# Optimization experiments

Measured on AMD Instinct MI355X. Metric: run time of the kernel, lower is better.

## Reference

```python
import jax, jax.numpy as jnp
import numpy as np

B, T, D = 2, 4096, 512
H = 8
HD = D // H  # 64


def setup_inputs() -> dict:
    key = jax.random.key(0)
    k1, k2, k3 = jax.random.split(key, 3)
    x = jax.random.normal(k1, (B, T, D), dtype=jnp.float32)
    w_qkv = jax.random.normal(k2, (3 * D, D), dtype=jnp.float32) * (1.0 / np.sqrt(D))
    w_out = jax.random.normal(k3, (D, D), dtype=jnp.float32) * (1.0 / np.sqrt(D))
    return {"x": x, "w_qkv": w_qkv, "w_out": w_out}


def reference(x, w_qkv, w_out):
    b, t, d = x.shape
    qkv = x @ w_qkv.T                      # [B,T,3D]
    q, k, v = jnp.split(qkv, 3, axis=-1)
    # b t (h d) -> b h t d
    def split_heads(a):
        return a.reshape(b, t, H, HD).transpose(0, 2, 1, 3)
    q, k, v = split_heads(q), split_heads(k), split_heads(v)
    scale = 1.0 / np.sqrt(HD).astype(np.float32)
    scores = jnp.einsum('bhqd,bhkd->bhqk', q, k) * scale  # [B,H,T,T]
    causal = jnp.tril(jnp.ones((t, t), dtype=bool))        # keep lower triangle
    scores = jnp.where(causal[None, None], scores, -jnp.inf)
    attn = jax.nn.softmax(scores, axis=-1)
    out = jnp.einsum('bhqk,bhkd->bhqd', attn, v)           # [B,H,T,HD]
    out = out.transpose(0, 2, 1, 3).reshape(b, t, d)       # b h t d -> b t (h d)
    return out @ w_out.T
```

## Files before the change

### kernel.cpp

```cpp
#include <hip/hip_runtime.h>
#include <hip/hip_bf16.h>

#define BB 2
#define TT 4096
#define DD 512
#define HH 8
#define HD 64
#define M_TOT (BB*TT)
#define N_QKV (3*DD)

typedef __attribute__((ext_vector_type(8))) __bf16 bf16x8;
typedef __attribute__((ext_vector_type(4))) float f32x4;

#define MFMA16(a,b,c) __builtin_amdgcn_mfma_f32_16x16x32_bf16((a),(b),(c),0,0,0)

#define SCALE_L2E 0.18033688011112443f
#define SHIFT_L2E 11.541560327111707f

static __device__ __forceinline__ unsigned short f2bf(float f) {
    union { float f; unsigned u; } v; v.f = f;
    return (unsigned short)((v.u + 0x8000u) >> 16);
}

static __device__ __forceinline__ bf16x8 load8(const unsigned short* p) {
    bf16x8 v;
    __builtin_memcpy(&v, p, 16);
    return v;
}

static __device__ __forceinline__ bf16x8 ones_frag() {
    unsigned short u[8];
    #pragma unroll
    for (int i = 0; i < 8; i++) u[i] = 0x3F80;
    bf16x8 v; __builtin_memcpy(&v, u, 16);
    return v;
}

#define GLDS(gp, lp) __builtin_amdgcn_global_load_lds( \
    (const __attribute__((address_space(1))) unsigned int*)(gp), \
    (__attribute__((address_space(3))) unsigned int*)(lp), 16, 0, 0)

#define NX4 (M_TOT*DD/4)
#define NW4 (N_QKV*DD/4)
#define NO4 (DD*DD/4)
__global__ __launch_bounds__(256) void cast_all(
        const float* __restrict__ x, const float* __restrict__ wqkv,
        const float* __restrict__ wout,
        unsigned short* __restrict__ xb, unsigned short* __restrict__ wqkvb,
        unsigned short* __restrict__ woutb) {
    int i = blockIdx.x * 256 + threadIdx.x;
    const float* s; unsigned short* d; int j;
    if (i < NX4)            { s = x;    d = xb;    j = i; }
    else if (i < NX4 + NW4) { s = wqkv; d = wqkvb; j = i - NX4; }
    else                    { s = wout; d = woutb; j = i - NX4 - NW4; }
    float4 f = ((const float4*)s)[j];
    ushort4 o;
    o.x = f2bf(f.x); o.y = f2bf(f.y); o.z = f2bf(f.z); o.w = f2bf(f.w);
    ((ushort4*)d)[j] = o;
}

__global__ __launch_bounds__(256) void qkv_gemm(
        const unsigned short* __restrict__ xb,
        const unsigned short* __restrict__ wb,
        unsigned short* __restrict__ qb,
        unsigned short* __restrict__ kb,
        unsigned short* __restrict__ vtb) {
    __shared__ unsigned short As[128 * 32];
    __shared__ unsigned short Bs[128 * 32];
    int tid = threadIdx.x;
    int w = tid >> 6, lane = tid & 63;
    int lrow = lane & 15, quad = lane >> 4;
    int bn = blockIdx.x % (N_QKV / 128);
    int bm = blockIdx.x / (N_QKV / 128);
    int m0 = bm * 128, n0 = bn * 128;
    int wm = w >> 1, wn = w & 1;

    f32x4 c[4][4];
    #pragma unroll
    for (int i = 0; i < 4; i++)
        #pragma unroll
        for (int j = 0; j < 4; j++) c[i][j] = (f32x4){0.f, 0.f, 0.f, 0.f};

    for (int k0 = 0; k0 < DD; k0 += 32) {
        #pragma unroll
        for (int j = 0; j < 2; j++) {
            int ch = j * 256 + tid;
            int row = ch >> 2, kc = ch & 3;
            GLDS(xb + (size_t)(m0 + row) * DD + k0 + kc * 8,
                 (char*)As + (size_t)(j * 256 + w * 64) * 16);
        }
        #pragma unroll
        for (int j = 0; j < 2; j++) {
            int ch = j * 256 + tid;
            int row = ch >> 2, kc = ch & 3;
            GLDS(wb + (size_t)(n0 + row) * DD + k0 + kc * 8,
                 (char*)Bs + (size_t)(j * 256 + w * 64) * 16);
        }
        __syncthreads();
        bf16x8 a[4], b[4];
        #pragma unroll
        for (int mf = 0; mf < 4; mf++) a[mf] = load8(&As[(wm * 64 + mf * 16 + lrow) * 32 + quad * 8]);
        #pragma unroll
        for (int nf = 0; nf < 4; nf++) b[nf] = load8(&Bs[(wn * 64 + nf * 16 + lrow) * 32 + quad * 8]);
        #pragma unroll
        for (int mf = 0; mf < 4; mf++)
            #pragma unroll
            for (int nf = 0; nf < 4; nf++)
                c[mf][nf] = MFMA16(a[mf], b[nf], c[mf][nf]);
        __syncthreads();
    }

    int m0w = m0 + wm * 64, n0w = n0 + wn * 64;
    int which = n0w >> 9;
    int h = (n0w & 511) >> 6;
    #pragma unroll
    for (int mf = 0; mf < 4; mf++) {
        #pragma unroll
        for (int r = 0; r < 4; r++) {
            int m = m0w + mf * 16 + quad * 4 + r;
            int t = m & (TT - 1), bi = m >> 12;
            size_t hb = (size_t)(bi * HH + h) * TT + t;
            #pragma unroll
            for (int nf = 0; nf < 4; nf++) {
                int d = nf * 16 + lrow;
                unsigned short val = f2bf(c[mf][nf][r]);
                if (which == 0)      qb[hb * HD + d] = val;
                else if (which == 1) kb[hb * HD + d] = val;
                else                 vtb[((size_t)(bi * HH + h) * HD + d) * TT + t] = val;
            }
        }
    }
}

__global__ __launch_bounds__(256) void attn_kernel(
        const unsigned short* __restrict__ qb,
        const unsigned short* __restrict__ kb,
        const unsigned short* __restrict__ vtb,
        unsigned short* __restrict__ attnb) {
    __shared__ union {
        unsigned short p[4][64][68];
        float c[2][64][66];
    } sm;

    int w = threadIdx.x >> 6;
    int lane = threadIdx.x & 63;
    int lrow = lane & 15, quad = lane >> 4;
    int bh = blockIdx.x & 15;
    int pr = blockIdx.x >> 4;
    int bi = bh >> 3, h = bh & 7;

    const unsigned short* qh = qb + (size_t)bh * TT * HD;
    const unsigned short* kh = kb + (size_t)bh * TT * HD;
    const unsigned short* vth = vtb + (size_t)bh * HD * TT;
    bf16x8 ones = ones_frag();

    for (int half = 0; half < 2; half++) {
        int qt = half ? (63 - pr) : pr;
        int q0 = qt * 64;

        bf16x8 qf[4][2];
        #pragma unroll
        for (int mf = 0; mf < 4; mf++) {
            const unsigned short* qp = qh + (q0 + mf * 16 + lrow) * HD + quad * 8;
            qf[mf][0] = load8(qp);
            qf[mf][1] = load8(qp + 32);
        }

        f32x4 o[4][4];
        f32x4 l[4];
        #pragma unroll
        for (int i = 0; i < 4; i++) {
            l[i] = (f32x4){0.f, 0.f, 0.f, 0.f};
            #pragma unroll
            for (int j = 0; j < 4; j++) o[i][j] = (f32x4){0.f, 0.f, 0.f, 0.f};
        }

        for (int kt = w; kt <= qt; kt += 4) {
            int kbase = kt * 64;
            bool diag = (kt == qt);
            #pragma unroll
            for (int nf = 0; nf < 4; nf++) {
                const unsigned short* kp = kh + (kbase + nf * 16 + lrow) * HD + quad * 8;
                bf16x8 kf0 = load8(kp);
                bf16x8 kf1 = load8(kp + 32);
                #pragma unroll
                for (int mf = 0; mf < 4; mf++) {
                    if (diag && nf > mf) {
                        #pragma unroll
                        for (int r = 0; r < 4; r++)
                            sm.p[w][mf * 16 + quad * 4 + r][nf * 16 + lrow] = 0;
                    } else {
                        f32x4 s = {0.f, 0.f, 0.f, 0.f};
                        s = MFMA16(qf[mf][0], kf0, s);
                        s = MFMA16(qf[mf][1], kf1, s);
                        #pragma unroll
                        for (int r = 0; r < 4; r++) {
                            float p = __builtin_amdgcn_exp2f(s[r] * SCALE_L2E - SHIFT_L2E);
                            if (diag && nf == mf && lrow > quad * 4 + r) p = 0.f;
                            sm.p[w][mf * 16 + quad * 4 + r][nf * 16 + lrow] = f2bf(p);
                        }
                    }
                }
            }
            bf16x8 vf[4][2];
            #pragma unroll
            for (int nfd = 0; nfd < 4; nfd++) {
                const unsigned short* vp = vth + (nfd * 16 + lrow) * TT + kbase + quad * 8;
                vf[nfd][0] = load8(vp);
                vf[nfd][1] = load8(vp + 32);
            }
            #pragma unroll
            for (int mf = 0; mf < 4; mf++) {
                bf16x8 pa0, pa1;
                __builtin_memcpy(&pa0, &sm.p[w][mf * 16 + lrow][quad * 8], 16);
                __builtin_memcpy(&pa1, &sm.p[w][mf * 16 + lrow][32 + quad * 8], 16);
                l[mf] = MFMA16(pa0, ones, l[mf]);
                l[mf] = MFMA16(pa1, ones, l[mf]);
                #pragma unroll
                for (int nfd = 0; nfd < 4; nfd++) {
                    o[mf][nfd] = MFMA16(pa0, vf[nfd][0], o[mf][nfd]);
                    o[mf][nfd] = MFMA16(pa1, vf[nfd][1], o[mf][nfd]);
                }
            }
        }

        __syncthreads();
        if (w >= 2) {
            int cb = w - 2;
            #pragma unroll
            for (int mf = 0; mf < 4; mf++)
                #pragma unroll
                for (int r = 0; r < 4; r++) {
                    int row = mf * 16 + quad * 4 + r;
                    #pragma unroll
                    for (int nfd = 0; nfd < 4; nfd++)
                        sm.c[cb][row][nfd * 16 + lrow] = o[mf][nfd][r];
                    if (lrow == 0) sm.c[cb][row][64] = l[mf][r];
                }
        }
        __syncthreads();
        if (w < 2) {
            #pragma unroll
            for (int mf = 0; mf < 4; mf++)
                #pragma unroll
                for (int r = 0; r < 4; r++) {
                    int row = mf * 16 + quad * 4 + r;
                    #pragma unroll
                    for (int nfd = 0; nfd < 4; nfd++)
                        sm.c[w][row][nfd * 16 + lrow] += o[mf][nfd][r];
                    if (lrow == 0) sm.c[w][row][64] += l[mf][r];
                }
        }
        __syncthreads();
        #pragma unroll
        for (int r = 0; r < 4; r++) {
            int row = w * 16 + quad * 4 + r;
            float lsum = sm.c[0][row][64] + sm.c[1][row][64];
            float inv = 1.0f / lsum;
            int t = q0 + row;
            size_t base = ((size_t)(bi * TT + t)) * DD + h * HD;
            #pragma unroll
            for (int nfd = 0; nfd < 4; nfd++) {
                int col = nfd * 16 + lrow;
                float v = (sm.c[0][row][col] + sm.c[1][row][col]) * inv;
                attnb[base + col] = f2bf(v);
            }
        }
        __syncthreads();
    }
}

__global__ __launch_bounds__(256) void proj_gemm(
        const unsigned short* __restrict__ ab,
        const unsigned short* __restrict__ wb,
        float* __restrict__ out) {
    __shared__ unsigned short As[128 * 32];
    __shared__ unsigned short Bs[128 * 32];
    int tid = threadIdx.x;
    int w = tid >> 6, lane = tid & 63;
    int lrow = lane & 15, quad = lane >> 4;
    int bn = blockIdx.x % (DD / 128);
    int bm = blockIdx.x / (DD / 128);
    int m0 = bm * 128, n0 = bn * 128;
    int wm = w >> 1, wn = w & 1;

    f32x4 c[4][4];
    #pragma unroll
    for (int i = 0; i < 4; i++)
        #pragma unroll
        for (int j = 0; j < 4; j++) c[i][j] = (f32x4){0.f, 0.f, 0.f, 0.f};

    for (int k0 = 0; k0 < DD; k0 += 32) {
        #pragma unroll
        for (int j = 0; j < 2; j++) {
            int ch = j * 256 + tid;
            int row = ch >> 2, kc = ch & 3;
            GLDS(ab + (size_t)(m0 + row) * DD + k0 + kc * 8,
                 (char*)As + (size_t)(j * 256 + w * 64) * 16);
        }
        #pragma unroll
        for (int j = 0; j < 2; j++) {
            int ch = j * 256 + tid;
            int row = ch >> 2, kc = ch & 3;
            GLDS(wb + (size_t)(n0 + row) * DD + k0 + kc * 8,
                 (char*)Bs + (size_t)(j * 256 + w * 64) * 16);
        }
        __syncthreads();
        bf16x8 a[4], b[4];
        #pragma unroll
        for (int mf = 0; mf < 4; mf++) a[mf] = load8(&As[(wm * 64 + mf * 16 + lrow) * 32 + quad * 8]);
        #pragma unroll
        for (int nf = 0; nf < 4; nf++) b[nf] = load8(&Bs[(wn * 64 + nf * 16 + lrow) * 32 + quad * 8]);
        #pragma unroll
        for (int mf = 0; mf < 4; mf++)
            #pragma unroll
            for (int nf = 0; nf < 4; nf++)
                c[mf][nf] = MFMA16(a[mf], b[nf], c[mf][nf]);
        __syncthreads();
    }

    #pragma unroll
    for (int mf = 0; mf < 4; mf++) {
        #pragma unroll
        for (int r = 0; r < 4; r++) {
            int m = m0 + wm * 64 + mf * 16 + quad * 4 + r;
            #pragma unroll
            for (int nf = 0; nf < 4; nf++) {
                int n = n0 + wn * 64 + nf * 16 + lrow;
                out[(size_t)m * DD + n] = c[mf][nf][r];
            }
        }
    }
}

extern "C" void kernel_launch(void* const* d_in, const int* in_sizes, int n_in,
                              void* d_out, int out_size, void* d_ws, size_t ws_size,
                              hipStream_t stream) {
    const float* x    = (const float*)d_in[0];
    const float* wqkv = (const float*)d_in[1];
    const float* wout = (const float*)d_in[2];
    float* out = (float*)d_out;

    char* ws = (char*)d_ws;
    unsigned short* xb    = (unsigned short*)ws; ws += (size_t)M_TOT * DD * 2;
    unsigned short* wqkvb = (unsigned short*)ws; ws += (size_t)N_QKV * DD * 2;
    unsigned short* woutb = (unsigned short*)ws; ws += (size_t)DD * DD * 2;
    unsigned short* qb    = (unsigned short*)ws; ws += (size_t)BB * HH * TT * HD * 2;
    unsigned short* kb    = (unsigned short*)ws; ws += (size_t)BB * HH * TT * HD * 2;
    unsigned short* vtb   = (unsigned short*)ws; ws += (size_t)BB * HH * HD * TT * 2;
    unsigned short* attnb = (unsigned short*)ws; ws += (size_t)M_TOT * DD * 2;

    cast_all<<<(NX4 + NW4 + NO4) / 256, 256, 0, stream>>>(x, wqkv, wout, xb, wqkvb, woutb);

    qkv_gemm<<<(M_TOT / 128) * (N_QKV / 128), 256, 0, stream>>>(xb, wqkvb, qb, kb, vtb);

    attn_kernel<<<512, 256, 0, stream>>>(qb, kb, vtb, attnb);

    proj_gemm<<<(M_TOT / 128) * (DD / 128), 256, 0, stream>>>(attnb, woutb, out);
}
```

Before: 190.6 us.

## Widen attention to six waves, deepen GEMM K-tile, truncate bf16 rounding

```diff
diff --git a/kernel.cpp b/kernel.cpp
--- a/kernel.cpp
+++ b/kernel.cpp
@@ -20,6 +20,10 @@
 static __device__ __forceinline__ unsigned short f2bf(float f) {
     union { float f; unsigned u; } v; v.f = f;
     return (unsigned short)((v.u + 0x8000u) >> 16);
+}
+static __device__ __forceinline__ unsigned short f2bf_t(float f) {
+    union { float f; unsigned u; } v; v.f = f;
+    return (unsigned short)(v.u >> 16);
 }
 
 static __device__ __forceinline__ bf16x8 load8(const unsigned short* p) {
@@ -65,8 +69,8 @@
         unsigned short* __restrict__ qb,
         unsigned short* __restrict__ kb,
         unsigned short* __restrict__ vtb) {
-    __shared__ unsigned short As[128 * 32];
-    __shared__ unsigned short Bs[128 * 32];
+    __shared__ unsigned short As[128 * 64];
+    __shared__ unsigned short Bs[128 * 64];
     int tid = threadIdx.x;
     int w = tid >> 6, lane = tid & 63;
     int lrow = lane & 15, quad = lane >> 4;
@@ -81,32 +85,37 @@
         #pragma unroll
         for (int j = 0; j < 4; j++) c[i][j] = (f32x4){0.f, 0.f, 0.f, 0.f};
 
-    for (int k0 = 0; k0 < DD; k0 += 32) {
-        #pragma unroll
-        for (int j = 0; j < 2; j++) {
+    for (int k0 = 0; k0 < DD; k0 += 64) {
+        #pragma unroll
+        for (int j = 0; j < 4; j++) {
             int ch = j * 256 + tid;
-            int row = ch >> 2, kc = ch & 3;
+            int row = ch >> 3, kc = ch & 7;
             GLDS(xb + (size_t)(m0 + row) * DD + k0 + kc * 8,
                  (char*)As + (size_t)(j * 256 + w * 64) * 16);
         }
         #pragma unroll
-        for (int j = 0; j < 2; j++) {
+        for (int j = 0; j < 4; j++) {
             int ch = j * 256 + tid;
-            int row = ch >> 2, kc = ch & 3;
+            int row = ch >> 3, kc = ch & 7;
             GLDS(wb + (size_t)(n0 + row) * DD + k0 + kc * 8,
                  (char*)Bs + (size_t)(j * 256 + w * 64) * 16);
         }
         __syncthreads();
-        bf16x8 a[4], b[4];
-        #pragma unroll
-        for (int mf = 0; mf < 4; mf++) a[mf] = load8(&As[(wm * 64 + mf * 16 + lrow) * 32 + quad * 8]);
-        #pragma unroll
-        for (int nf = 0; nf < 4; nf++) b[nf] = load8(&Bs[(wn * 64 + nf * 16 + lrow) * 32 + quad * 8]);
-        #pragma unroll
-        for (int mf = 0; mf < 4; mf++)
+        #pragma unroll
+        for (int kc = 0; kc < 2; kc++) {
+            bf16x8 a[4], b[4];
+            #pragma unroll
+            for (int mf = 0; mf < 4; mf++)
+                a[mf] = load8(&As[(wm * 64 + mf * 16 + lrow) * 64 + kc * 32 + quad * 8]);
             #pragma unroll
             for (int nf = 0; nf < 4; nf++)
-                c[mf][nf] = MFMA16(a[mf], b[nf], c[mf][nf]);
+                b[nf] = load8(&Bs[(wn * 64 + nf * 16 + lrow) * 64 + kc * 32 + quad * 8]);
+            #pragma unroll
+            for (int mf = 0; mf < 4; mf++)
+                #pragma unroll
+                for (int nf = 0; nf < 4; nf++)
+                    c[mf][nf] = MFMA16(a[mf], b[nf], c[mf][nf]);
+        }
         __syncthreads();
     }
 
@@ -132,14 +141,14 @@
     }
 }
 
-__global__ __launch_bounds__(256) void attn_kernel(
+__global__ __launch_bounds__(384, 3) void attn_kernel(
         const unsigned short* __restrict__ qb,
         const unsigned short* __restrict__ kb,
         const unsigned short* __restrict__ vtb,
         unsigned short* __restrict__ attnb) {
     __shared__ union {
-        unsigned short p[4][64][68];
-        float c[2][64][66];
+        unsigned short p[6][64][68];
+        float c[3][64][66];
     } sm;
 
     int w = threadIdx.x >> 6;
@@ -175,7 +184,7 @@
             for (int j = 0; j < 4; j++) o[i][j] = (f32x4){0.f, 0.f, 0.f, 0.f};
         }
 
-        for (int kt = w; kt <= qt; kt += 4) {
+        for (int kt = w; kt <= qt; kt += 6) {
             int kbase = kt * 64;
             bool diag = (kt == qt);
             #pragma unroll
@@ -197,7 +206,7 @@
                         for (int r = 0; r < 4; r++) {
                             float p = __builtin_amdgcn_exp2f(s[r] * SCALE_L2E - SHIFT_L2E);
                             if (diag && nf == mf && lrow > quad * 4 + r) p = 0.f;
-                            sm.p[w][mf * 16 + quad * 4 + r][nf * 16 + lrow] = f2bf(p);
+                            sm.p[w][mf * 16 + quad * 4 + r][nf * 16 + lrow] = f2bf_t(p);
                         }
                     }
                 }
@@ -225,8 +234,8 @@
         }
 
         __syncthreads();
-        if (w >= 2) {
-            int cb = w - 2;
+        if (w >= 3) {
+            int cb = w - 3;
             #pragma unroll
             for (int mf = 0; mf < 4; mf++)
                 #pragma unroll
@@ -239,7 +248,7 @@
                 }
         }
         __syncthreads();
-        if (w < 2) {
+        if (w < 3) {
             #pragma unroll
             for (int mf = 0; mf < 4; mf++)
                 #pragma unroll
@@ -252,18 +261,20 @@
                 }
         }
         __syncthreads();
-        #pragma unroll
-        for (int r = 0; r < 4; r++) {
-            int row = w * 16 + quad * 4 + r;
-            float lsum = sm.c[0][row][64] + sm.c[1][row][64];
-            float inv = 1.0f / lsum;
-            int t = q0 + row;
-            size_t base = ((size_t)(bi * TT + t)) * DD + h * HD;
-            #pragma unroll
-            for (int nfd = 0; nfd < 4; nfd++) {
-                int col = nfd * 16 + lrow;
-                float v = (sm.c[0][row][col] + sm.c[1][row][col]) * inv;
-                attnb[base + col] = f2bf(v);
+        if (w < 4) {
+            #pragma unroll
+            for (int r = 0; r < 4; r++) {
+                int row = w * 16 + quad * 4 + r;
+                float lsum = sm.c[0][row][64] + sm.c[1][row][64] + sm.c[2][row][64];
+                float inv = 1.0f / lsum;
+                int t = q0 + row;
+                size_t base = ((size_t)(bi * TT + t)) * DD + h * HD;
+                #pragma unroll
+                for (int nfd = 0; nfd < 4; nfd++) {
+                    int col = nfd * 16 + lrow;
+                    float v = (sm.c[0][row][col] + sm.c[1][row][col] + sm.c[2][row][col]) * inv;
+                    attnb[base + col] = f2bf_t(v);
+                }
             }
         }
         __syncthreads();
@@ -274,8 +285,8 @@
         const unsigned short* __restrict__ ab,
         const unsigned short* __restrict__ wb,
         float* __restrict__ out) {
-    __shared__ unsigned short As[128 * 32];
-    __shared__ unsigned short Bs[128 * 32];
+    __shared__ unsigned short As[128 * 64];
+    __shared__ unsigned short Bs[128 * 64];
     int tid = threadIdx.x;
     int w = tid >> 6, lane = tid & 63;
     int lrow = lane & 15, quad = lane >> 4;
@@ -290,32 +301,37 @@
         #pragma unroll
         for (int j = 0; j < 4; j++) c[i][j] = (f32x4){0.f, 0.f, 0.f, 0.f};
 
-    for (int k0 = 0; k0 < DD; k0 += 32) {
-        #pragma unroll
-        for (int j = 0; j < 2; j++) {
+    for (int k0 = 0; k0 < DD; k0 += 64) {
+        #pragma unroll
+        for (int j = 0; j < 4; j++) {
             int ch = j * 256 + tid;
-            int row = ch >> 2, kc = ch & 3;
+            int row = ch >> 3, kc = ch & 7;
             GLDS(ab + (size_t)(m0 + row) * DD + k0 + kc * 8,
                  (char*)As + (size_t)(j * 256 + w * 64) * 16);
         }
         #pragma unroll
-        for (int j = 0; j < 2; j++) {
+        for (int j = 0; j < 4; j++) {
             int ch = j * 256 + tid;
-            int row = ch >> 2, kc = ch & 3;
+            int row = ch >> 3, kc = ch & 7;
             GLDS(wb + (size_t)(n0 + row) * DD + k0 + kc * 8,
                  (char*)Bs + (size_t)(j * 256 + w * 64) * 16);
         }
         __syncthreads();
-        bf16x8 a[4], b[4];
-        #pragma unroll
-        for (int mf = 0; mf < 4; mf++) a[mf] = load8(&As[(wm * 64 + mf * 16 + lrow) * 32 + quad * 8]);
-        #pragma unroll
-        for (int nf = 0; nf < 4; nf++) b[nf] = load8(&Bs[(wn * 64 + nf * 16 + lrow) * 32 + quad * 8]);
-        #pragma unroll
-        for (int mf = 0; mf < 4; mf++)
+        #pragma unroll
+        for (int kc = 0; kc < 2; kc++) {
+            bf16x8 a[4], b[4];
+            #pragma unroll
+            for (int mf = 0; mf < 4; mf++)
+                a[mf] = load8(&As[(wm * 64 + mf * 16 + lrow) * 64 + kc * 32 + quad * 8]);
             #pragma unroll
             for (int nf = 0; nf < 4; nf++)
-                c[mf][nf] = MFMA16(a[mf], b[nf], c[mf][nf]);
+                b[nf] = load8(&Bs[(wn * 64 + nf * 16 + lrow) * 64 + kc * 32 + quad * 8]);
+            #pragma unroll
+            for (int mf = 0; mf < 4; mf++)
+                #pragma unroll
+                for (int nf = 0; nf < 4; nf++)
+                    c[mf][nf] = MFMA16(a[mf], b[nf], c[mf][nf]);
+        }
         __syncthreads();
     }
 
@@ -354,7 +370,7 @@
 
     qkv_gemm<<<(M_TOT / 128) * (N_QKV / 128), 256, 0, stream>>>(xb, wqkvb, qb, kb, vtb);
 
-    attn_kernel<<<512, 256, 0, stream>>>(qb, kb, vtb, attnb);
+    attn_kernel<<<512, 384, 0, stream>>>(qb, kb, vtb, attnb);
 
     proj_gemm<<<(M_TOT / 128) * (DD / 128), 256, 0, stream>>>(attnb, woutb, out);
 }
```

After: 256.2 us. 1.34x slower.

## Coalesce V-transpose and attention output stores, reorder K/V loads, shrink proj tiles

Applied to the files above, without the earlier changes.

```diff
diff --git a/kernel.cpp b/kernel.cpp
--- a/kernel.cpp
+++ b/kernel.cpp
@@ -12,7 +12,7 @@
 typedef __attribute__((ext_vector_type(8))) __bf16 bf16x8;
 typedef __attribute__((ext_vector_type(4))) float f32x4;
 
-#define MFMA16(a,b,c) __builtin_amdgcn_mfma_f32_16x16x32_bf16((a),(b),(c),0,0,0)
+#define MFMA32(a,b,c) __builtin_amdgcn_mfma_f32_16x16x32_bf16((a),(b),(c),0,0,0)
 
 #define SCALE_L2E 0.18033688011112443f
 #define SHIFT_L2E 11.541560327111707f
@@ -20,6 +20,10 @@
 static __device__ __forceinline__ unsigned short f2bf(float f) {
     union { float f; unsigned u; } v; v.f = f;
     return (unsigned short)((v.u + 0x8000u) >> 16);
+}
+static __device__ __forceinline__ unsigned short f2bf_t(float f) {
+    union { float f; unsigned u; } v; v.f = f;
+    return (unsigned short)(v.u >> 16);
 }
 
 static __device__ __forceinline__ bf16x8 load8(const unsigned short* p) {
@@ -65,8 +69,10 @@
         unsigned short* __restrict__ qb,
         unsigned short* __restrict__ kb,
         unsigned short* __restrict__ vtb) {
-    __shared__ unsigned short As[128 * 32];
-    __shared__ unsigned short Bs[128 * 32];
+    __shared__ union {
+        struct { unsigned short As[128 * 32]; unsigned short Bs[128 * 32]; } g;
+        unsigned short vt[4][64][72];
+    } sm;
     int tid = threadIdx.x;
     int w = tid >> 6, lane = tid & 63;
     int lrow = lane & 15, quad = lane >> 4;
@@ -87,47 +93,63 @@
             int ch = j * 256 + tid;
             int row = ch >> 2, kc = ch & 3;
             GLDS(xb + (size_t)(m0 + row) * DD + k0 + kc * 8,
-                 (char*)As + (size_t)(j * 256 + w * 64) * 16);
+                 (char*)sm.g.As + (size_t)(j * 256 + w * 64) * 16);
         }
         #pragma unroll
         for (int j = 0; j < 2; j++) {
             int ch = j * 256 + tid;
             int row = ch >> 2, kc = ch & 3;
             GLDS(wb + (size_t)(n0 + row) * DD + k0 + kc * 8,
-                 (char*)Bs + (size_t)(j * 256 + w * 64) * 16);
+                 (char*)sm.g.Bs + (size_t)(j * 256 + w * 64) * 16);
         }
         __syncthreads();
         bf16x8 a[4], b[4];
         #pragma unroll
-        for (int mf = 0; mf < 4; mf++) a[mf] = load8(&As[(wm * 64 + mf * 16 + lrow) * 32 + quad * 8]);
-        #pragma unroll
-        for (int nf = 0; nf < 4; nf++) b[nf] = load8(&Bs[(wn * 64 + nf * 16 + lrow) * 32 + quad * 8]);
+        for (int mf = 0; mf < 4; mf++) a[mf] = load8(&sm.g.As[(wm * 64 + mf * 16 + lrow) * 32 + quad * 8]);
+        #pragma unroll
+        for (int nf = 0; nf < 4; nf++) b[nf] = load8(&sm.g.Bs[(wn * 64 + nf * 16 + lrow) * 32 + quad * 8]);
         #pragma unroll
         for (int mf = 0; mf < 4; mf++)
             #pragma unroll
             for (int nf = 0; nf < 4; nf++)
-                c[mf][nf] = MFMA16(a[mf], b[nf], c[mf][nf]);
+                c[mf][nf] = MFMA32(a[mf], b[nf], c[mf][nf]);
         __syncthreads();
     }
 
     int m0w = m0 + wm * 64, n0w = n0 + wn * 64;
     int which = n0w >> 9;
     int h = (n0w & 511) >> 6;
-    #pragma unroll
-    for (int mf = 0; mf < 4; mf++) {
-        #pragma unroll
-        for (int r = 0; r < 4; r++) {
-            int m = m0w + mf * 16 + quad * 4 + r;
-            int t = m & (TT - 1), bi = m >> 12;
-            size_t hb = (size_t)(bi * HH + h) * TT + t;
-            #pragma unroll
-            for (int nf = 0; nf < 4; nf++) {
-                int d = nf * 16 + lrow;
-                unsigned short val = f2bf(c[mf][nf][r]);
-                if (which == 0)      qb[hb * HD + d] = val;
-                else if (which == 1) kb[hb * HD + d] = val;
-                else                 vtb[((size_t)(bi * HH + h) * HD + d) * TT + t] = val;
-            }
+    if (which < 2) {
+        unsigned short* dst = (which == 0) ? qb : kb;
+        #pragma unroll
+        for (int mf = 0; mf < 4; mf++) {
+            #pragma unroll
+            for (int r = 0; r < 4; r++) {
+                int m = m0w + mf * 16 + quad * 4 + r;
+                int t = m & (TT - 1), bi = m >> 12;
+                size_t hb = (size_t)(bi * HH + h) * TT + t;
+                #pragma unroll
+                for (int nf = 0; nf < 4; nf++)
+                    dst[hb * HD + nf * 16 + lrow] = f2bf(c[mf][nf][r]);
+            }
+        }
+    } else {
+        #pragma unroll
+        for (int mf = 0; mf < 4; mf++)
+            #pragma unroll
+            for (int r = 0; r < 4; r++)
+                #pragma unroll
+                for (int nf = 0; nf < 4; nf++)
+                    sm.vt[w][nf * 16 + lrow][mf * 16 + quad * 4 + r] = f2bf(c[mf][nf][r]);
+        int bi = m0w >> 12, t0 = m0w & (TT - 1);
+        size_t hb = (size_t)(bi * HH + h) * HD;
+        #pragma unroll
+        for (int i = 0; i < 8; i++) {
+            int d = i * 8 + (lane >> 3);
+            int tc = (lane & 7) * 8;
+            bf16x8 v;
+            __builtin_memcpy(&v, &sm.vt[w][d][tc], 16);
+            __builtin_memcpy(vtb + (hb + d) * TT + t0 + tc, &v, 16);
         }
     }
 }
@@ -142,6 +164,7 @@
         float c[2][64][66];
     } sm;
 
+    const f32x4 ZERO4 = {0.f, 0.f, 0.f, 0.f};
     int w = threadIdx.x >> 6;
     int lane = threadIdx.x & 63;
     int lrow = lane & 15, quad = lane >> 4;
@@ -170,56 +193,52 @@
         f32x4 l[4];
         #pragma unroll
         for (int i = 0; i < 4; i++) {
-            l[i] = (f32x4){0.f, 0.f, 0.f, 0.f};
-            #pragma unroll
-            for (int j = 0; j < 4; j++) o[i][j] = (f32x4){0.f, 0.f, 0.f, 0.f};
+            l[i] = ZERO4;
+            #pragma unroll
+            for (int j = 0; j < 4; j++) o[i][j] = ZERO4;
         }
 
         for (int kt = w; kt <= qt; kt += 4) {
             int kbase = kt * 64;
             bool diag = (kt == qt);
+            bf16x8 kf[4][2], vf[4][2];
             #pragma unroll
             for (int nf = 0; nf < 4; nf++) {
                 const unsigned short* kp = kh + (kbase + nf * 16 + lrow) * HD + quad * 8;
-                bf16x8 kf0 = load8(kp);
-                bf16x8 kf1 = load8(kp + 32);
-                #pragma unroll
-                for (int mf = 0; mf < 4; mf++) {
+                kf[nf][0] = load8(kp);
+                kf[nf][1] = load8(kp + 32);
+                const unsigned short* vp = vth + (nf * 16 + lrow) * TT + kbase + quad * 8;
+                vf[nf][0] = load8(vp);
+                vf[nf][1] = load8(vp + 32);
+            }
+            #pragma unroll
+            for (int mf = 0; mf < 4; mf++) {
+                #pragma unroll
+                for (int nf = 0; nf < 4; nf++) {
                     if (diag && nf > mf) {
                         #pragma unroll
                         for (int r = 0; r < 4; r++)
                             sm.p[w][mf * 16 + quad * 4 + r][nf * 16 + lrow] = 0;
                     } else {
-                        f32x4 s = {0.f, 0.f, 0.f, 0.f};
-                        s = MFMA16(qf[mf][0], kf0, s);
-                        s = MFMA16(qf[mf][1], kf1, s);
+                        f32x4 s = MFMA32(qf[mf][0], kf[nf][0], ZERO4);
+                        s = MFMA32(qf[mf][1], kf[nf][1], s);
                         #pragma unroll
                         for (int r = 0; r < 4; r++) {
                             float p = __builtin_amdgcn_exp2f(s[r] * SCALE_L2E - SHIFT_L2E);
                             if (diag && nf == mf && lrow > quad * 4 + r) p = 0.f;
-                            sm.p[w][mf * 16 + quad * 4 + r][nf * 16 + lrow] = f2bf(p);
+                            sm.p[w][mf * 16 + quad * 4 + r][nf * 16 + lrow] = f2bf_t(p);
                         }
                     }
                 }
-            }
-            bf16x8 vf[4][2];
-            #pragma unroll
-            for (int nfd = 0; nfd < 4; nfd++) {
-                const unsigned short* vp = vth + (nfd * 16 + lrow) * TT + kbase + quad * 8;
-                vf[nfd][0] = load8(vp);
-                vf[nfd][1] = load8(vp + 32);
-            }
-            #pragma unroll
-            for (int mf = 0; mf < 4; mf++) {
                 bf16x8 pa0, pa1;
                 __builtin_memcpy(&pa0, &sm.p[w][mf * 16 + lrow][quad * 8], 16);
                 __builtin_memcpy(&pa1, &sm.p[w][mf * 16 + lrow][32 + quad * 8], 16);
-                l[mf] = MFMA16(pa0, ones, l[mf]);
-                l[mf] = MFMA16(pa1, ones, l[mf]);
+                l[mf] = MFMA32(pa0, ones, l[mf]);
+                l[mf] = MFMA32(pa1, ones, l[mf]);
                 #pragma unroll
                 for (int nfd = 0; nfd < 4; nfd++) {
-                    o[mf][nfd] = MFMA16(pa0, vf[nfd][0], o[mf][nfd]);
-                    o[mf][nfd] = MFMA16(pa1, vf[nfd][1], o[mf][nfd]);
+                    o[mf][nfd] = MFMA32(pa0, vf[nfd][0], o[mf][nfd]);
+                    o[mf][nfd] = MFMA32(pa1, vf[nfd][1], o[mf][nfd]);
                 }
             }
         }
@@ -252,19 +271,21 @@
                 }
         }
         __syncthreads();
-        #pragma unroll
-        for (int r = 0; r < 4; r++) {
-            int row = w * 16 + quad * 4 + r;
-            float lsum = sm.c[0][row][64] + sm.c[1][row][64];
-            float inv = 1.0f / lsum;
-            int t = q0 + row;
-            size_t base = ((size_t)(bi * TT + t)) * DD + h * HD;
-            #pragma unroll
-            for (int nfd = 0; nfd < 4; nfd++) {
-                int col = nfd * 16 + lrow;
-                float v = (sm.c[0][row][col] + sm.c[1][row][col]) * inv;
-                attnb[base + col] = f2bf(v);
-            }
+        {
+            int q = threadIdx.x >> 2, dseg = (threadIdx.x & 3) * 16;
+            const float* r0 = &sm.c[0][q][0];
+            const float* r1 = &sm.c[1][q][0];
+            float inv = 1.0f / (r0[64] + r1[64]);
+            unsigned outp[8];
+            #pragma unroll
+            for (int i = 0; i < 8; i++) {
+                float a0 = (r0[dseg + 2 * i] + r1[dseg + 2 * i]) * inv;
+                float a1 = (r0[dseg + 2 * i + 1] + r1[dseg + 2 * i + 1]) * inv;
+                outp[i] = (unsigned)f2bf_t(a0) | ((unsigned)f2bf_t(a1) << 16);
+            }
+            unsigned short* dst = attnb + ((size_t)(bi * TT + q0 + q)) * DD + h * HD + dseg;
+            __builtin_memcpy(dst, outp, 16);
+            __builtin_memcpy(dst + 8, outp + 4, 16);
         }
         __syncthreads();
     }
@@ -274,29 +295,27 @@
         const unsigned short* __restrict__ ab,
         const unsigned short* __restrict__ wb,
         float* __restrict__ out) {
-    __shared__ unsigned short As[128 * 32];
+    __shared__ unsigned short As[64 * 32];
     __shared__ unsigned short Bs[128 * 32];
     int tid = threadIdx.x;
     int w = tid >> 6, lane = tid & 63;
     int lrow = lane & 15, quad = lane >> 4;
     int bn = blockIdx.x % (DD / 128);
     int bm = blockIdx.x / (DD / 128);
-    int m0 = bm * 128, n0 = bn * 128;
-    int wm = w >> 1, wn = w & 1;
-
-    f32x4 c[4][4];
+    int m0 = bm * 64, n0 = bn * 128;
+
+    f32x4 c[4][2];
     #pragma unroll
     for (int i = 0; i < 4; i++)
         #pragma unroll
-        for (int j = 0; j < 4; j++) c[i][j] = (f32x4){0.f, 0.f, 0.f, 0.f};
+        for (int j = 0; j < 2; j++) c[i][j] = (f32x4){0.f, 0.f, 0.f, 0.f};
 
     for (int k0 = 0; k0 < DD; k0 += 32) {
-        #pragma unroll
-        for (int j = 0; j < 2; j++) {
-            int ch = j * 256 + tid;
+        {
+            int ch = tid;
             int row = ch >> 2, kc = ch & 3;
             GLDS(ab + (size_t)(m0 + row) * DD + k0 + kc * 8,
-                 (char*)As + (size_t)(j * 256 + w * 64) * 16);
+                 (char*)As + (size_t)(w * 64) * 16);
         }
         #pragma unroll
         for (int j = 0; j < 2; j++) {
@@ -306,16 +325,16 @@
                  (char*)Bs + (size_t)(j * 256 + w * 64) * 16);
         }
         __syncthreads();
-        bf16x8 a[4], b[4];
-        #pragma unroll
-        for (int mf = 0; mf < 4; mf++) a[mf] = load8(&As[(wm * 64 + mf * 16 + lrow) * 32 + quad * 8]);
-        #pragma unroll
-        for (int nf = 0; nf < 4; nf++) b[nf] = load8(&Bs[(wn * 64 + nf * 16 + lrow) * 32 + quad * 8]);
+        bf16x8 a[4], b[2];
+        #pragma unroll
+        for (int mf = 0; mf < 4; mf++) a[mf] = load8(&As[(mf * 16 + lrow) * 32 + quad * 8]);
+        #pragma unroll
+        for (int nf = 0; nf < 2; nf++) b[nf] = load8(&Bs[(w * 32 + nf * 16 + lrow) * 32 + quad * 8]);
         #pragma unroll
         for (int mf = 0; mf < 4; mf++)
             #pragma unroll
-            for (int nf = 0; nf < 4; nf++)
-                c[mf][nf] = MFMA16(a[mf], b[nf], c[mf][nf]);
+            for (int nf = 0; nf < 2; nf++)
+                c[mf][nf] = MFMA32(a[mf], b[nf], c[mf][nf]);
         __syncthreads();
     }
 
@@ -323,10 +342,10 @@
     for (int mf = 0; mf < 4; mf++) {
         #pragma unroll
         for (int r = 0; r < 4; r++) {
-            int m = m0 + wm * 64 + mf * 16 + quad * 4 + r;
-            #pragma unroll
-            for (int nf = 0; nf < 4; nf++) {
-                int n = n0 + wn * 64 + nf * 16 + lrow;
+            int m = m0 + mf * 16 + quad * 4 + r;
+            #pragma unroll
+            for (int nf = 0; nf < 2; nf++) {
+                int n = n0 + w * 32 + nf * 16 + lrow;
                 out[(size_t)m * DD + n] = c[mf][nf][r];
             }
         }
@@ -356,5 +375,5 @@
 
     attn_kernel<<<512, 256, 0, stream>>>(qb, kb, vtb, attnb);
 
-    proj_gemm<<<(M_TOT / 128) * (DD / 128), 256, 0, stream>>>(attnb, woutb, out);
-}
+    proj_gemm<<<(M_TOT / 64) * (DD / 128), 256, 0, stream>>>(attnb, woutb, out);
+}
```

After: 176.8 us. 1.08x faster.
